# Performance work log

Hardware: AMD Instinct MI355X
Metric: run time of the kernel (lower is better)

## Reference

```python
import jax, jax.numpy as jnp
import numpy as np
from jax import lax

B, N, CIN, MID, OUT, G, H, CHILDS = 16, 1024, 256, 512, 256, 4, 1, 512


def _ln(x, g, b, eps=1e-6):
    m = x.mean(-1, keepdims=True)
    v = ((x - m) ** 2).mean(-1, keepdims=True)
    return (x - m) / jnp.sqrt(v + eps) * g + b


def _gconv(x, W, b):
    # grouped 1x1 conv1d: x [B,Cin,N], W [Cout, Cin//G], b [Cout]
    Bb, Cin, Nn = x.shape
    Cout = W.shape[0]
    xg = x.reshape(Bb, G, Cin // G, Nn)
    Wg = W.reshape(G, Cout // G, Cin // G)
    y = jnp.einsum('bgcn,goc->bgon', xg, Wg).reshape(Bb, Cout, Nn)
    return y + b[None, :, None]


def _forward(x, masks_roi1, masks_roi2, score_mask, gt_feat,
             W_att, b_att, W1, b1, W2, b2, g1, beta1, g2, beta2, Wg, bg):
    dt = x.dtype
    # gt branch
    gts = jax.nn.relu(gt_feat @ Wg + bg)  # [B,N,OUT]

    mr1 = masks_roi1 * score_mask[:, None, :]
    mr2 = masks_roi2 * score_mask[:, None, :]

    # attention logits without materializing the [B,N,N,2C] concat:
    # ft[b,i,j] = cat(x[b,j], x[b,i]);  logits = ft @ W_att + b_att
    Wq, Wk = W_att[:CIN], W_att[CIN:]
    lj = jnp.einsum('bjc,ch->bjh', x, Wq)  # query part (varies over j)
    li = jnp.einsum('bic,ch->bih', x, Wk)  # key part   (varies over i)
    attn = jax.nn.sigmoid(lj[:, None, :, :] + li[:, :, None, :] + b_att)  # [B,N,N,H]

    attn1 = attn * mr1[:, :, :, None]
    attn2 = attn * mr2[:, :, :, None]

    # torch fancy-index assign atten_mask[:,:,idces,:]=1 reduces to: any column
    # index appearing in ANY topk index set gets 1 along dim 2 for all b,i,h.
    k4, k2 = CHILDS // 4, CHILDS // 2
    a1 = jnp.moveaxis(attn1, 2, 3)  # [B,N,H,N] -> topk over last axis (= dim 2)
    a2 = jnp.moveaxis(attn2, 2, 3)
    idx1 = lax.top_k(a1, k4)[1]
    idx1m = lax.top_k(-a1, k4)[1]
    idx2 = lax.top_k(a2, k2)[1]
    idx2m = lax.top_k(-a2, k4)[1]
    all_idx = jnp.concatenate([idx1.ravel(), idx1m.ravel(), idx2.ravel(), idx2m.ravel()])
    col = jnp.zeros((N,), dtype=dt).at[all_idx].set(1.0)

    attn = attn * (mr1 + mr2)[:, :, :, None] * col[None, None, :, None]

    f = (score_mask == 0).astype(dt)  # [B,N]
    f_diag = f[:, :, None] * jnp.eye(N, dtype=dt)  # diag_embed
    atten = (attn + f_diag[:, :, :, None]) / CHILDS
    atten = jnp.transpose(atten, (0, 3, 2, 1))  # [B,H,Nj,Ni]

    x_t = jnp.transpose(x, (0, 2, 1))  # [B,CIN,N]
    o1 = jax.nn.relu(_gconv(x_t, W1, b1))  # [B,MID,N]
    o1m = jnp.matmul(o1.reshape(B, H, MID // H, N), atten).reshape(B, MID, N)
    o1m = _ln(jnp.transpose(o1m, (0, 2, 1)), g1, beta1)  # [B,N,MID]
    o1 = o1 + jnp.transpose(o1m, (0, 2, 1))

    o2 = jax.nn.relu(_gconv(o1, W2, b2))  # [B,OUT,N]
    o2m = jnp.matmul(o2.reshape(B, H, OUT // H, N), atten).reshape(B, OUT, N)
    node_feat = _ln(jnp.transpose(o2m, (0, 2, 1)), g2, beta2)  # [B,N,OUT]
    o2 = o2 + jnp.transpose(node_feat, (0, 2, 1))
    output2 = jnp.transpose(o2, (0, 2, 1))  # [B,N,OUT]
    return output2, gts, node_feat


def setup_inputs() -> dict:
    key = jax.random.key(0)
    ks = jax.random.split(key, 16)
    x = jax.random.normal(ks[0], (B, N, CIN), jnp.float32)
    masks_roi1 = (jax.random.uniform(ks[1], (B, N, N)) < 0.1).astype(jnp.float32)
    masks_roi2 = (jax.random.uniform(ks[2], (B, N, N)) < 0.1).astype(jnp.float32)
    score_mask = (jax.random.uniform(ks[3], (B, N)) < 0.8).astype(jnp.float32)
    gt_feat = jax.random.normal(ks[4], (B, N, CIN), jnp.float32)
    s = 0.05
    W_att = jax.random.normal(ks[5], (2 * CIN, H), jnp.float32) * s
    b_att = jnp.zeros((H,), jnp.float32)
    W1 = jax.random.normal(ks[6], (MID, CIN // G), jnp.float32) * s
    b1 = jax.random.normal(ks[7], (MID,), jnp.float32) * s
    W2 = jax.random.normal(ks[8], (OUT, MID // G), jnp.float32) * s
    b2 = jax.random.normal(ks[9], (OUT,), jnp.float32) * s
    g1 = jax.random.normal(ks[10], (MID,), jnp.float32) * s
    beta1 = jnp.zeros((MID,), jnp.float32)
    g2 = jax.random.normal(ks[11], (OUT,), jnp.float32) * s
    beta2 = jnp.zeros((OUT,), jnp.float32)
    Wg = jax.random.normal(ks[12], (CIN, OUT), jnp.float32) * s
    bg = jax.random.normal(ks[13], (OUT,), jnp.float32) * s
    return {"x": x, "masks_roi1": masks_roi1, "masks_roi2": masks_roi2,
            "score_mask": score_mask, "gt_feat": gt_feat,
            "W_att": W_att, "b_att": b_att, "W1": W1, "b1": b1,
            "W2": W2, "b2": b2, "g1": g1, "beta1": beta1,
            "g2": g2, "beta2": beta2, "Wg": Wg, "bg": bg}


def reference(x, masks_roi1, masks_roi2, score_mask, gt_feat,
              W_att, b_att, W1, b1, W2, b2, g1, beta1, g2, beta2, Wg, bg):
    return _forward(x, masks_roi1, masks_roi2, score_mask, gt_feat,
                    W_att, b_att, W1, b1, W2, b2, g1, beta1, g2, beta2, Wg, bg)
```

## Files before the change

kernel.cpp:

```cpp
#include <hip/hip_runtime.h>
#include <cstddef>
#include <cstdint>

#define B_ 16
#define N_ 1024
#define CIN_ 256
#define MID_ 512
#define OUT_ 256

typedef __attribute__((ext_vector_type(8))) short short8v;
typedef __attribute__((ext_vector_type(4))) float f32x4;

__device__ __forceinline__ float sigf(float z){ return 1.f/(1.f+expf(-z)); }
__device__ __forceinline__ ushort f2bf(float f){
  uint32_t u=__float_as_uint(f);
  uint32_t r=(u + 0x7fffu + ((u>>16)&1u))>>16;
  return (ushort)r;
}
__device__ __forceinline__ float bf2f(ushort u){ return __uint_as_float(((uint32_t)u)<<16); }

__device__ __forceinline__ void async16(void* lds, const void* g){
  __builtin_amdgcn_global_load_lds(
      (const __attribute__((address_space(1))) uint32_t*)g,
      (__attribute__((address_space(3))) uint32_t*)lds,
      16, 0, 0);
}

__global__ __launch_bounds__(256) void k_pc(const float* __restrict__ x,
    const float* __restrict__ gt, const float* __restrict__ Watt,
    float* __restrict__ lj, float* __restrict__ li,
    ushort* __restrict__ xb, ushort* __restrict__ gtb)
{
  int bid=blockIdx.x, wid=threadIdx.x>>6, lane=threadIdx.x&63;
  if(bid < 4096){
    int row = bid*4 + wid;
    float4 xv = ((const float4*)(x + (size_t)row*CIN_))[lane];
    ((ushort4*)(xb + (size_t)row*CIN_))[lane] =
        make_ushort4(f2bf(xv.x), f2bf(xv.y), f2bf(xv.z), f2bf(xv.w));
    float4 q = ((const float4*)Watt)[lane];
    float4 w = ((const float4*)(Watt + CIN_))[lane];
    float aq = xv.x*q.x+xv.y*q.y+xv.z*q.z+xv.w*q.w;
    float ak = xv.x*w.x+xv.y*w.y+xv.z*w.z+xv.w*w.w;
    #pragma unroll
    for(int off=32; off; off>>=1){ aq += __shfl_xor(aq,off); ak += __shfl_xor(ak,off); }
    if(lane==0){ lj[row]=aq; li[row]=ak; }
  } else {
    int row = (bid-4096)*4 + wid;
    float4 v = ((const float4*)(gt + (size_t)row*CIN_))[lane];
    ((ushort4*)(gtb + (size_t)row*CIN_))[lane] =
        make_ushort4(f2bf(v.x), f2bf(v.y), f2bf(v.z), f2bf(v.w));
  }
}

__global__ __launch_bounds__(256) void k_wcast(const float* __restrict__ W1,
    const float* __restrict__ W2, const float* __restrict__ Wg,
    ushort* __restrict__ W1b, ushort* __restrict__ W2b, ushort* __restrict__ WgTb)
{
  int bid=blockIdx.x, t=threadIdx.x;
  if(bid<128){ int i=bid*256+t; W1b[i]=f2bf(W1[i]); }
  else if(bid<256){ int i=(bid-128)*256+t; W2b[i]=f2bf(W2[i]); }
  else { int idx=(bid-256)*256+t; int o=idx>>8, c=idx&255; WgTb[idx]=f2bf(Wg[(size_t)c*OUT_+o]); }
}

__global__ __launch_bounds__(256) void k_col(
    const float* __restrict__ m1, const float* __restrict__ m2,
    const float* __restrict__ sc, const float* __restrict__ lj,
    const float* __restrict__ li, const float* __restrict__ batt,
    float* __restrict__ colf, ushort* __restrict__ mrs)
{
  int row = blockIdx.x; int b = row >> 10; int t = threadIdx.x;
  int lane = t&63, wid = t>>6;
  size_t base = (size_t)row*N_ + 4*t;
  float4 m1v = *(const float4*)(m1 + base);
  float4 m2v = *(const float4*)(m2 + base);
  float4 scv = *(const float4*)(sc + (b<<10) + 4*t);
  float mr1[4] = {m1v.x*scv.x, m1v.y*scv.y, m1v.z*scv.z, m1v.w*scv.w};
  float mr2[4] = {m2v.x*scv.x, m2v.y*scv.y, m2v.z*scv.z, m2v.w*scv.w};
  *(ushort4*)(mrs + base) = make_ushort4(f2bf(mr1[0]+mr2[0]), f2bf(mr1[1]+mr2[1]),
                                         f2bf(mr1[2]+mr2[2]), f2bf(mr1[3]+mr2[3]));
  int z1=0,z2=0;
  #pragma unroll
  for(int k=0;k<4;++k){ z1 += (mr1[k]==0.f); z2 += (mr2[k]==0.f); }
  int s = z1 | (z2<<16);
  #pragma unroll
  for(int off=1; off<64; off<<=1){
    int u = __shfl_up(s,off);
    if(lane>=off) s += u;
  }
  __shared__ int wsum[4];
  if(lane==63) wsum[wid]=s;
  __syncthreads();
  int prev=0, tot=0;
  #pragma unroll
  for(int w2=0;w2<4;++w2){ int v=wsum[w2]; tot+=v; if(w2<wid) prev+=v; }
  int incl = s + prev;
  int z1i = incl & 0xffff, z2i = incl >> 16;
  int excl1 = z1i - z1, excl2 = z2i - z2;
  int Z1 = tot & 0xffff, Z2 = tot >> 16;
  int P1 = 1024-Z1, P2 = 1024-Z2;
  bool rare = (P1>128)||(P2>256)||(Z1<128)||(Z2<128);
  if(!rare){
    int zb1=excl1, zb2=excl2;
    #pragma unroll
    for(int k=0;k<4;++k){
      bool q = (mr1[k]!=0.f) || (zb1<128) || (mr2[k]!=0.f) || (zb2<128) || (P2+zb2<256);
      if(q) colf[4*t+k]=1.0f;
      zb1 += (mr1[k]==0.f); zb2 += (mr2[k]==0.f);
    }
  } else {
    float lir=li[row], ba=batt[0];
    const float* m1r = m1 + (size_t)row*N_;
    const float* m2r = m2 + (size_t)row*N_;
    const float* scr = sc + (b<<10);
    const float* ljr = lj + (b<<10);
    float a1v[4], a2v[4];
    #pragma unroll
    for(int k=0;k<4;++k){
      float v = sigf(ljr[4*t+k]+lir+ba);
      a1v[k]=mr1[k]*v; a2v[k]=mr2[k]*v;
    }
    int c1[4]={0,0,0,0}, c1m[4]={0,0,0,0}, c2[4]={0,0,0,0}, c2m[4]={0,0,0,0};
    for(int jp=0;jp<N_;++jp){
      float vv = sigf(ljr[jp]+lir+ba);
      float p1 = m1r[jp]*scr[jp]*vv, p2 = m2r[jp]*scr[jp]*vv;
      #pragma unroll
      for(int k=0;k<4;++k){
        bool lo = jp < 4*t+k;
        c1[k] += (p1>a1v[k])||((p1==a1v[k])&&lo);
        c1m[k]+= (p1<a1v[k])||((p1==a1v[k])&&lo);
        c2[k] += (p2>a2v[k])||((p2==a2v[k])&&lo);
        c2m[k]+= (p2<a2v[k])||((p2==a2v[k])&&lo);
      }
    }
    #pragma unroll
    for(int k=0;k<4;++k)
      if(c1[k]<128||c1m[k]<128||c2[k]<256||c2m[k]<128) colf[4*t+k]=1.0f;
  }
}

__global__ __launch_bounds__(256) void k_at(const ushort* __restrict__ mrs,
    const float* __restrict__ sc, const float* __restrict__ lj,
    const float* __restrict__ li, const float* __restrict__ batt,
    const float* __restrict__ colf, ushort* __restrict__ Atb)
{
  int row=blockIdx.x, t=threadIdx.x; int b=row>>10, i=row&1023;
  size_t base=(size_t)row*N_ + 4*t;
  ushort4 mv=*(const ushort4*)(mrs+base);
  float4 ljv=*(const float4*)(lj + (b<<10) + 4*t);
  float4 cv =*(const float4*)(colf + 4*t);
  float lir=li[row], ba=batt[0];
  float fi = (sc[(b<<10)+i]==0.f)?1.f:0.f;
  float mra[4]={bf2f(mv.x),bf2f(mv.y),bf2f(mv.z),bf2f(mv.w)};
  float ljr[4]={ljv.x,ljv.y,ljv.z,ljv.w};
  float cr[4]={cv.x,cv.y,cv.z,cv.w};
  ushort o[4]; int j0=4*t;
  #pragma unroll
  for(int k=0;k<4;++k){
    float v=sigf(ljr[k]+lir+ba);
    float val=v*mra[k]*cr[k];
    if(j0+k==i) val+=fi;
    o[k]=f2bf(val*(1.f/512.f));
  }
  *(ushort4*)(Atb+base) = make_ushort4(o[0],o[1],o[2],o[3]);
}

template<int BM,int BN,int WR,int WC,int BK>
__global__ __launch_bounds__(256) void mgemm(
    const ushort* __restrict__ A, int lda, long long sAb, long long sAg,
    const ushort* __restrict__ Bp, int ldb, long long sBb, long long sBg,
    float* __restrict__ C, ushort* __restrict__ Cb, int ldc, long long sCb, long long sCg,
    ushort* __restrict__ CbT, long long sTb, long long sTg, int ldt,
    int K, int nG,
    const float* __restrict__ biasM, int biasMG,
    const float* __restrict__ biasN, int relu)
{
  static_assert(WR*WC==4 && BM==WR*64 && BN==WC*64, "tile");
  static_assert((BM*BK)%512==0 && (BN*BK)%512==0, "stage align");
  __shared__ __align__(16) ushort As[BM*BK];
  __shared__ __align__(16) ushort Bs[BN*BK];
  int z=blockIdx.z, b=z/nG, g=z%nG;
  A  += (size_t)b*sAb + (size_t)g*sAg;
  Bp += (size_t)b*sBb + (size_t)g*sBg;
  size_t cOff = (size_t)b*sCb + (size_t)g*sCg;
  size_t tOff = (size_t)b*sTb + (size_t)g*sTg;
  int m0 = blockIdx.y*BM, n0 = blockIdx.x*BN;
  int tid=threadIdx.x, w=tid>>6, lane=tid&63;
  int la=lane&15, hi=lane>>4;
  int wr=w/WC, wc=w%WC;
  f32x4 acc[4][4] = {};
  constexpr int ISS = (BM+BN)*BK/2048;
  for(int k0=0;k0<K;k0+=BK){
    #pragma unroll
    for(int r=0;r<ISS;++r){
      int e = (r*256 + tid)*8;
      if(e < BM*BK){
        int row=e/BK, kk=e%BK;
        async16((char*)As + (size_t)e*2, A + (size_t)(m0+row)*lda + k0+kk);
      } else {
        int e2=e-BM*BK; int row=e2/BK, kk=e2%BK;
        async16((char*)Bs + (size_t)e2*2, Bp + (size_t)(n0+row)*ldb + k0+kk);
      }
    }
    __syncthreads();
    #pragma unroll
    for(int h=0;h<BK/32;++h){
      short8v af[4], bf4[4];
      #pragma unroll
      for(int i2=0;i2<4;++i2) af[i2] = *(const short8v*)&As[(wr*64+i2*16+la)*BK + h*32 + hi*8];
      #pragma unroll
      for(int j2=0;j2<4;++j2) bf4[j2] = *(const short8v*)&Bs[(wc*64+j2*16+la)*BK + h*32 + hi*8];
      #pragma unroll
      for(int i2=0;i2<4;++i2)
        #pragma unroll
        for(int j2=0;j2<4;++j2)
          acc[i2][j2] = __builtin_amdgcn_mfma_f32_16x16x32_bf16(af[i2], bf4[j2], acc[i2][j2], 0,0,0);
    }
    __syncthreads();
  }
  #pragma unroll
  for(int i2=0;i2<4;++i2){
    int row0 = m0 + wr*64 + i2*16 + hi*4;
    #pragma unroll
    for(int j2=0;j2<4;++j2){
      int col = n0 + wc*64 + j2*16 + la;
      float bn = biasN ? biasN[col] : 0.f;
      #pragma unroll
      for(int r=0;r<4;++r){
        int row = row0 + r;
        float v = acc[i2][j2][r] + bn + (biasM ? biasM[(size_t)g*biasMG + row] : 0.f);
        if(relu) v = fmaxf(v, 0.f);
        if(C)   C  [cOff + (size_t)row*ldc + col] = v;
        if(Cb)  Cb [cOff + (size_t)row*ldc + col] = f2bf(v);
        if(CbT) CbT[tOff + (size_t)col*ldt + row] = f2bf(v);
      }
    }
  }
}

__global__ __launch_bounds__(256) void k_ln1(const float* __restrict__ o1mT,
    const ushort* __restrict__ o1bT,
    const float* __restrict__ g1v, const float* __restrict__ be1, ushort* __restrict__ o1pb)
{
  int row=blockIdx.x, t=threadIdx.x;
  float2 v = ((const float2*)(o1mT + (size_t)row*MID_))[t];
  float s=v.x+v.y, s2=v.x*v.x+v.y*v.y;
  for(int off=32; off; off>>=1){ s+=__shfl_down(s,off); s2+=__shfl_down(s2,off); }
  __shared__ float sm[8];
  int lane=t&63, wid=t>>6;
  if(lane==0){ sm[wid]=s; sm[4+wid]=s2; }
  __syncthreads();
  s=sm[0]+sm[1]+sm[2]+sm[3]; s2=sm[4]+sm[5]+sm[6]+sm[7];
  float mean=s*(1.f/MID_), var=s2*(1.f/MID_)-mean*mean;
  float rstd=rsqrtf(var+1e-6f);
  int m0=2*t;
  float a0=(v.x-mean)*rstd*g1v[m0]+be1[m0];
  float a1=(v.y-mean)*rstd*g1v[m0+1]+be1[m0+1];
  ushort2 rr = ((const ushort2*)(o1bT + (size_t)row*MID_))[t];
  ushort2 o; o.x=f2bf(a0+bf2f(rr.x)); o.y=f2bf(a1+bf2f(rr.y));
  ((ushort2*)(o1pb + (size_t)row*MID_))[t] = o;
}

__global__ __launch_bounds__(256) void k_ln2f(const float* __restrict__ o2mT,
    const ushort* __restrict__ o2bT,
    const float* __restrict__ g2v, const float* __restrict__ be2,
    float* __restrict__ node, float* __restrict__ out2)
{
  int row=blockIdx.x, t=threadIdx.x;
  float v = o2mT[(size_t)row*OUT_ + t];
  float s=v, s2=v*v;
  for(int off=32; off; off>>=1){ s+=__shfl_down(s,off); s2+=__shfl_down(s2,off); }
  __shared__ float sm[8];
  int lane=t&63, wid=t>>6;
  if(lane==0){ sm[wid]=s; sm[4+wid]=s2; }
  __syncthreads();
  s=sm[0]+sm[1]+sm[2]+sm[3]; s2=sm[4]+sm[5]+sm[6]+sm[7];
  float mean=s*(1.f/OUT_); float var=s2*(1.f/OUT_)-mean*mean;
  float rstd=rsqrtf(var+1e-6f);
  float nf=(v-mean)*rstd*g2v[t]+be2[t];
  size_t ro=(size_t)row*OUT_+t;
  node[ro]=nf;
  out2[ro]=nf + bf2f(o2bT[ro]);
}

extern "C" void kernel_launch(void* const* d_in, const int* in_sizes, int n_in,
                              void* d_out, int out_size, void* d_ws, size_t ws_size,
                              hipStream_t stream)
{
  const float* x    = (const float*)d_in[0];
  const float* m1   = (const float*)d_in[1];
  const float* m2   = (const float*)d_in[2];
  const float* sc   = (const float*)d_in[3];
  const float* gt   = (const float*)d_in[4];
  const float* Watt = (const float*)d_in[5];
  const float* batt = (const float*)d_in[6];
  const float* W1   = (const float*)d_in[7];
  const float* b1   = (const float*)d_in[8];
  const float* W2   = (const float*)d_in[9];
  const float* b2   = (const float*)d_in[10];
  const float* g1   = (const float*)d_in[11];
  const float* be1  = (const float*)d_in[12];
  const float* g2   = (const float*)d_in[13];
  const float* be2  = (const float*)d_in[14];
  const float* Wg   = (const float*)d_in[15];
  const float* bg   = (const float*)d_in[16];

  float* out2 = (float*)d_out;
  float* gtso = out2 + (size_t)B_*N_*OUT_;
  float* node = gtso + (size_t)B_*N_*OUT_;

  char* ws = (char*)d_ws;
  float*  colf = (float*)(ws);
  float*  lj   = (float*)(ws + 4096);
  float*  li   = (float*)(ws + 69632);
  ushort* W1b  = (ushort*)(ws + 135168);
  ushort* W2b  = (ushort*)(ws + 200704);
  ushort* WgTb = (ushort*)(ws + 266240);
  char* R1 = ws + 1048576;
  ushort* mrs  = (ushort*)R1;
  float*  o1mT = (float*)R1;
  ushort* Atb  = (ushort*)(ws + 34603008);
  char* R3 = ws + 68157440;
  ushort* xb   = (ushort*)R3;
  ushort* gtb  = (ushort*)(R3 + 8388608);
  ushort* o2b  = (ushort*)R3;
  ushort* o2bT = (ushort*)(R3 + 8388608);
  char* R4 = ws + 84934656;
  ushort* o1b  = (ushort*)R4;
  ushort* o1pb = (ushort*)R4;
  char* R5 = ws + 101711872;
  ushort* o1bT = (ushort*)R5;
  float*  o2mT = (float*)R5;

  hipMemsetAsync(colf, 0, 4096, stream);
  k_pc   <<<dim3(8192),dim3(256),0,stream>>>(x, gt, Watt, lj, li, xb, gtb);
  k_wcast<<<dim3(512),dim3(256),0,stream>>>(W1, W2, Wg, W1b, W2b, WgTb);
  k_col  <<<dim3(B_*N_),dim3(256),0,stream>>>(m1,m2,sc,lj,li,batt,colf,mrs);
  k_at   <<<dim3(B_*N_),dim3(256),0,stream>>>(mrs,sc,lj,li,batt,colf,Atb);

  mgemm<128,128,2,2,64><<<dim3(2,128,1),256,0,stream>>>(
      gtb, CIN_, 0,0,
      WgTb, CIN_, 0,0,
      gtso, (ushort*)0, OUT_, 0,0,
      (ushort*)0, 0,0,0,
      CIN_, 1, nullptr,0, bg, 1);

  mgemm<128,128,2,2,64><<<dim3(8,1,B_*4),256,0,stream>>>(
      W1b, 64, 0, (long long)128*64,
      xb, CIN_, (long long)N_*CIN_, 64,
      (float*)0, o1b, N_, (long long)MID_*N_, (long long)128*N_,
      o1bT, (long long)N_*MID_, 128, MID_,
      64, 4, b1, 128, nullptr, 1);

  mgemm<128,128,2,2,64><<<dim3(4,8,B_),256,0,stream>>>(
      Atb, N_, (long long)N_*N_, 0,
      o1b, N_, (long long)MID_*N_, 0,
      o1mT, (ushort*)0, MID_, (long long)N_*MID_, 0,
      (ushort*)0, 0,0,0,
      N_, 1, nullptr,0, nullptr, 0);

  k_ln1<<<dim3(B_*N_),256,0,stream>>>(o1mT, o1bT, g1, be1, o1pb);

  mgemm<64,256,1,4,64><<<dim3(4,1,B_*4),256,0,stream>>>(
      W2b, 128, 0, (long long)64*128,
      o1pb, MID_, (long long)N_*MID_, 128,
      (float*)0, o2b, N_, (long long)OUT_*N_, (long long)64*N_,
      o2bT, (long long)N_*OUT_, 64, OUT_,
      128, 4, b2, 64, nullptr, 1);

  mgemm<128,128,2,2,64><<<dim3(2,8,B_),256,0,stream>>>(
      Atb, N_, (long long)N_*N_, 0,
      o2b, N_, (long long)OUT_*N_, 0,
      o2mT, (ushort*)0, OUT_, (long long)N_*OUT_, 0,
      (ushort*)0, 0,0,0,
      N_, 1, nullptr,0, nullptr, 0);

  k_ln2f<<<dim3(B_*N_),256,0,stream>>>(o2mT, o2bT, g2, be2, node, out2);
}
```

Before: 398.4 us.

## Fuse column-mask and attention kernels, apply column mask in GEMM epilogue

Merges k_col and k_at into one pass that writes the attention matrix without the column factor. The column selection is now recorded as per-row ballot bitmasks, which a small kernel OR-reduces. The column mask is applied afterwards by zeroing the masked columns of the o1b/o2b operands in the producing GEMM epilogues, and the diagonal term for masked columns is corrected in the attention GEMM epilogue. This removes the intermediate mrs array, one full pass over the 16M-element mask rows, and the colf memset. The attention GEMM outputs are also stored as bf16 instead of fp32, which halves their write and read traffic but adds rounding error before the layer norms.

```diff
diff --git a/kernel.cpp b/kernel.cpp
--- a/kernel.cpp
+++ b/kernel.cpp
@@ -10,6 +10,7 @@
 
 typedef __attribute__((ext_vector_type(8))) short short8v;
 typedef __attribute__((ext_vector_type(4))) float f32x4;
+typedef unsigned long long ull;
 
 __device__ __forceinline__ float sigf(float z){ return 1.f/(1.f+expf(-z)); }
 __device__ __forceinline__ ushort f2bf(float f){
@@ -24,6 +25,10 @@
       (const __attribute__((address_space(1))) uint32_t*)g,
       (__attribute__((address_space(3))) uint32_t*)lds,
       16, 0, 0);
+}
+
+__device__ __forceinline__ int colbit(const ull* __restrict__ cm, int j){
+  return (int)((cm[((j>>8)<<2) | (j&3)] >> ((j>>2)&63)) & 1ull);
 }
 
 __global__ __launch_bounds__(256) void k_pc(const float* __restrict__ x,
@@ -62,66 +67,77 @@
   else { int idx=(bid-256)*256+t; int o=idx>>8, c=idx&255; WgTb[idx]=f2bf(Wg[(size_t)c*OUT_+o]); }
 }
 
-__global__ __launch_bounds__(256) void k_col(
+__global__ __launch_bounds__(256) void k_colat(
     const float* __restrict__ m1, const float* __restrict__ m2,
     const float* __restrict__ sc, const float* __restrict__ lj,
     const float* __restrict__ li, const float* __restrict__ batt,
-    float* __restrict__ colf, ushort* __restrict__ mrs)
-{
-  int row = blockIdx.x; int b = row >> 10; int t = threadIdx.x;
-  int lane = t&63, wid = t>>6;
+    ushort* __restrict__ Atb, ull* __restrict__ blockmask)
+{
+  int row = blockIdx.x; int b = row >> 10; int i = row & 1023;
+  int t = threadIdx.x, lane = t&63, wid = t>>6;
   size_t base = (size_t)row*N_ + 4*t;
   float4 m1v = *(const float4*)(m1 + base);
   float4 m2v = *(const float4*)(m2 + base);
   float4 scv = *(const float4*)(sc + (b<<10) + 4*t);
+  float4 ljv = *(const float4*)(lj + (b<<10) + 4*t);
+  float lir = li[row], ba = batt[0];
+  float fi = (sc[(b<<10)+i]==0.f)?1.f:0.f;
   float mr1[4] = {m1v.x*scv.x, m1v.y*scv.y, m1v.z*scv.z, m1v.w*scv.w};
   float mr2[4] = {m2v.x*scv.x, m2v.y*scv.y, m2v.z*scv.z, m2v.w*scv.w};
-  *(ushort4*)(mrs + base) = make_ushort4(f2bf(mr1[0]+mr2[0]), f2bf(mr1[1]+mr2[1]),
-                                         f2bf(mr1[2]+mr2[2]), f2bf(mr1[3]+mr2[3]));
-  int z1=0,z2=0;
+  float ljr[4] = {ljv.x,ljv.y,ljv.z,ljv.w};
+  ushort o[4];
   #pragma unroll
-  for(int k=0;k<4;++k){ z1 += (mr1[k]==0.f); z2 += (mr2[k]==0.f); }
-  int s = z1 | (z2<<16);
+  for(int k=0;k<4;++k){
+    float v = sigf(ljr[k]+lir+ba);
+    float val = v*(mr1[k]+mr2[k]);
+    if(4*t+k==i) val += fi;
+    o[k] = f2bf(val*(1.f/512.f));
+  }
+  *(ushort4*)(Atb+base) = make_ushort4(o[0],o[1],o[2],o[3]);
+  ull zb1m0=__ballot(mr1[0]==0.f), zb1m1=__ballot(mr1[1]==0.f),
+      zb1m2=__ballot(mr1[2]==0.f), zb1m3=__ballot(mr1[3]==0.f);
+  ull zb2m0=__ballot(mr2[0]==0.f), zb2m1=__ballot(mr2[1]==0.f),
+      zb2m2=__ballot(mr2[2]==0.f), zb2m3=__ballot(mr2[3]==0.f);
+  int wz1 = __popcll(zb1m0)+__popcll(zb1m1)+__popcll(zb1m2)+__popcll(zb1m3);
+  int wz2 = __popcll(zb2m0)+__popcll(zb2m1)+__popcll(zb2m2)+__popcll(zb2m3);
+  __shared__ int wz[8];
+  if(lane==0){ wz[wid]=wz1; wz[4+wid]=wz2; }
+  __syncthreads();
+  int pre1=0, pre2=0, Z1=0, Z2=0;
   #pragma unroll
-  for(int off=1; off<64; off<<=1){
-    int u = __shfl_up(s,off);
-    if(lane>=off) s += u;
-  }
-  __shared__ int wsum[4];
-  if(lane==63) wsum[wid]=s;
-  __syncthreads();
-  int prev=0, tot=0;
-  #pragma unroll
-  for(int w2=0;w2<4;++w2){ int v=wsum[w2]; tot+=v; if(w2<wid) prev+=v; }
-  int incl = s + prev;
-  int z1i = incl & 0xffff, z2i = incl >> 16;
-  int excl1 = z1i - z1, excl2 = z2i - z2;
-  int Z1 = tot & 0xffff, Z2 = tot >> 16;
+  for(int w2=0;w2<4;++w2){
+    Z1 += wz[w2]; Z2 += wz[4+w2];
+    if(w2<wid){ pre1 += wz[w2]; pre2 += wz[4+w2]; }
+  }
+  ull lt = (1ull<<lane)-1ull;
+  int r1 = pre1 + __popcll(zb1m0&lt)+__popcll(zb1m1&lt)+__popcll(zb1m2&lt)+__popcll(zb1m3&lt);
+  int r2 = pre2 + __popcll(zb2m0&lt)+__popcll(zb2m1&lt)+__popcll(zb2m2&lt)+__popcll(zb2m3&lt);
   int P1 = 1024-Z1, P2 = 1024-Z2;
   bool rare = (P1>128)||(P2>256)||(Z1<128)||(Z2<128);
+  bool q0,q1,q2,q3;
   if(!rare){
-    int zb1=excl1, zb2=excl2;
-    #pragma unroll
-    for(int k=0;k<4;++k){
-      bool q = (mr1[k]!=0.f) || (zb1<128) || (mr2[k]!=0.f) || (zb2<128) || (P2+zb2<256);
-      if(q) colf[4*t+k]=1.0f;
-      zb1 += (mr1[k]==0.f); zb2 += (mr2[k]==0.f);
-    }
+    int zb1=r1, zb2=r2;
+    q0 = (mr1[0]!=0.f)||(zb1<128)||(mr2[0]!=0.f)||(zb2<128)||(P2+zb2<256);
+    zb1 += (int)((zb1m0>>lane)&1ull); zb2 += (int)((zb2m0>>lane)&1ull);
+    q1 = (mr1[1]!=0.f)||(zb1<128)||(mr2[1]!=0.f)||(zb2<128)||(P2+zb2<256);
+    zb1 += (int)((zb1m1>>lane)&1ull); zb2 += (int)((zb2m1>>lane)&1ull);
+    q2 = (mr1[2]!=0.f)||(zb1<128)||(mr2[2]!=0.f)||(zb2<128)||(P2+zb2<256);
+    zb1 += (int)((zb1m2>>lane)&1ull); zb2 += (int)((zb2m2>>lane)&1ull);
+    q3 = (mr1[3]!=0.f)||(zb1<128)||(mr2[3]!=0.f)||(zb2<128)||(P2+zb2<256);
   } else {
-    float lir=li[row], ba=batt[0];
     const float* m1r = m1 + (size_t)row*N_;
     const float* m2r = m2 + (size_t)row*N_;
     const float* scr = sc + (b<<10);
-    const float* ljr = lj + (b<<10);
+    const float* ljp = lj + (b<<10);
     float a1v[4], a2v[4];
     #pragma unroll
     for(int k=0;k<4;++k){
-      float v = sigf(ljr[4*t+k]+lir+ba);
+      float v = sigf(ljp[4*t+k]+lir+ba);
       a1v[k]=mr1[k]*v; a2v[k]=mr2[k]*v;
     }
     int c1[4]={0,0,0,0}, c1m[4]={0,0,0,0}, c2[4]={0,0,0,0}, c2m[4]={0,0,0,0};
     for(int jp=0;jp<N_;++jp){
-      float vv = sigf(ljr[jp]+lir+ba);
+      float vv = sigf(ljp[jp]+lir+ba);
       float p1 = m1r[jp]*scr[jp]*vv, p2 = m2r[jp]*scr[jp]*vv;
       #pragma unroll
       for(int k=0;k<4;++k){
@@ -132,36 +148,32 @@
         c2m[k]+= (p2<a2v[k])||((p2==a2v[k])&&lo);
       }
     }
-    #pragma unroll
-    for(int k=0;k<4;++k)
-      if(c1[k]<128||c1m[k]<128||c2[k]<256||c2m[k]<128) colf[4*t+k]=1.0f;
-  }
-}
-
-__global__ __launch_bounds__(256) void k_at(const ushort* __restrict__ mrs,
-    const float* __restrict__ sc, const float* __restrict__ lj,
-    const float* __restrict__ li, const float* __restrict__ batt,
-    const float* __restrict__ colf, ushort* __restrict__ Atb)
-{
-  int row=blockIdx.x, t=threadIdx.x; int b=row>>10, i=row&1023;
-  size_t base=(size_t)row*N_ + 4*t;
-  ushort4 mv=*(const ushort4*)(mrs+base);
-  float4 ljv=*(const float4*)(lj + (b<<10) + 4*t);
-  float4 cv =*(const float4*)(colf + 4*t);
-  float lir=li[row], ba=batt[0];
-  float fi = (sc[(b<<10)+i]==0.f)?1.f:0.f;
-  float mra[4]={bf2f(mv.x),bf2f(mv.y),bf2f(mv.z),bf2f(mv.w)};
-  float ljr[4]={ljv.x,ljv.y,ljv.z,ljv.w};
-  float cr[4]={cv.x,cv.y,cv.z,cv.w};
-  ushort o[4]; int j0=4*t;
+    q0 = (c1[0]<128||c1m[0]<128||c2[0]<256||c2m[0]<128);
+    q1 = (c1[1]<128||c1m[1]<128||c2[1]<256||c2m[1]<128);
+    q2 = (c1[2]<128||c1m[2]<128||c2[2]<256||c2m[2]<128);
+    q3 = (c1[3]<128||c1m[3]<128||c2[3]<256||c2m[3]<128);
+  }
+  ull bq0=__ballot(q0), bq1=__ballot(q1), bq2=__ballot(q2), bq3=__ballot(q3);
+  if(lane<4){
+    ull v = (lane==0)?bq0 : (lane==1)?bq1 : (lane==2)?bq2 : bq3;
+    blockmask[(size_t)(wid*4+lane)*16384 + row] = v;
+  }
+}
+
+__global__ __launch_bounds__(256) void k_colred(const ull* __restrict__ blockmask,
+    ull* __restrict__ colmask64)
+{
+  int w = blockIdx.x;
+  const ull* p = blockmask + (size_t)w*16384;
+  ull acc = 0;
+  for(int r=threadIdx.x; r<16384; r+=256) acc |= p[r];
   #pragma unroll
-  for(int k=0;k<4;++k){
-    float v=sigf(ljr[k]+lir+ba);
-    float val=v*mra[k]*cr[k];
-    if(j0+k==i) val+=fi;
-    o[k]=f2bf(val*(1.f/512.f));
-  }
-  *(ushort4*)(Atb+base) = make_ushort4(o[0],o[1],o[2],o[3]);
+  for(int off=32; off; off>>=1) acc |= __shfl_xor(acc, off);
+  __shared__ ull sm[4];
+  int lane=threadIdx.x&63, wid=threadIdx.x>>6;
+  if(lane==0) sm[wid]=acc;
+  __syncthreads();
+  if(threadIdx.x==0) colmask64[w] = sm[0]|sm[1]|sm[2]|sm[3];
 }
 
 template<int BM,int BN,int WR,int WC,int BK>
@@ -170,12 +182,13 @@
     const ushort* __restrict__ Bp, int ldb, long long sBb, long long sBg,
     float* __restrict__ C, ushort* __restrict__ Cb, int ldc, long long sCb, long long sCg,
     ushort* __restrict__ CbT, long long sTb, long long sTg, int ldt,
+    const ull* __restrict__ colmask, int scaleCb,
+    const ushort* __restrict__ corrT, long long sQb, int ldq, const float* __restrict__ scp,
     int K, int nG,
     const float* __restrict__ biasM, int biasMG,
     const float* __restrict__ biasN, int relu)
 {
   static_assert(WR*WC==4 && BM==WR*64 && BN==WC*64, "tile");
-  static_assert((BM*BK)%512==0 && (BN*BK)%512==0, "stage align");
   __shared__ __align__(16) ushort As[BM*BK];
   __shared__ __align__(16) ushort Bs[BN*BK];
   int z=blockIdx.z, b=z/nG, g=z%nG;
@@ -224,26 +237,32 @@
     for(int j2=0;j2<4;++j2){
       int col = n0 + wc*64 + j2*16 + la;
       float bn = biasN ? biasN[col] : 0.f;
+      float cs = (scaleCb && !colbit(colmask, col)) ? 0.f : 1.f;
       #pragma unroll
       for(int r=0;r<4;++r){
         int row = row0 + r;
         float v = acc[i2][j2][r] + bn + (biasM ? biasM[(size_t)g*biasMG + row] : 0.f);
+        if(corrT){
+          if(scp[(size_t)b*1024 + row]==0.f && !colbit(colmask, row))
+            v += (1.f/512.f)*bf2f(corrT[(size_t)b*sQb + (size_t)row*ldq + col]);
+        }
         if(relu) v = fmaxf(v, 0.f);
         if(C)   C  [cOff + (size_t)row*ldc + col] = v;
-        if(Cb)  Cb [cOff + (size_t)row*ldc + col] = f2bf(v);
+        if(Cb)  Cb [cOff + (size_t)row*ldc + col] = f2bf(v*cs);
         if(CbT) CbT[tOff + (size_t)col*ldt + row] = f2bf(v);
       }
     }
   }
 }
 
-__global__ __launch_bounds__(256) void k_ln1(const float* __restrict__ o1mT,
+__global__ __launch_bounds__(256) void k_ln1(const ushort* __restrict__ o1mTb,
     const ushort* __restrict__ o1bT,
     const float* __restrict__ g1v, const float* __restrict__ be1, ushort* __restrict__ o1pb)
 {
   int row=blockIdx.x, t=threadIdx.x;
-  float2 v = ((const float2*)(o1mT + (size_t)row*MID_))[t];
-  float s=v.x+v.y, s2=v.x*v.x+v.y*v.y;
+  ushort2 vv = ((const ushort2*)(o1mTb + (size_t)row*MID_))[t];
+  float vx=bf2f(vv.x), vy=bf2f(vv.y);
+  float s=vx+vy, s2=vx*vx+vy*vy;
   for(int off=32; off; off>>=1){ s+=__shfl_down(s,off); s2+=__shfl_down(s2,off); }
   __shared__ float sm[8];
   int lane=t&63, wid=t>>6;
@@ -253,20 +272,20 @@
   float mean=s*(1.f/MID_), var=s2*(1.f/MID_)-mean*mean;
   float rstd=rsqrtf(var+1e-6f);
   int m0=2*t;
-  float a0=(v.x-mean)*rstd*g1v[m0]+be1[m0];
-  float a1=(v.y-mean)*rstd*g1v[m0+1]+be1[m0+1];
+  float a0=(vx-mean)*rstd*g1v[m0]+be1[m0];
+  float a1=(vy-mean)*rstd*g1v[m0+1]+be1[m0+1];
   ushort2 rr = ((const ushort2*)(o1bT + (size_t)row*MID_))[t];
   ushort2 o; o.x=f2bf(a0+bf2f(rr.x)); o.y=f2bf(a1+bf2f(rr.y));
   ((ushort2*)(o1pb + (size_t)row*MID_))[t] = o;
 }
 
-__global__ __launch_bounds__(256) void k_ln2f(const float* __restrict__ o2mT,
+__global__ __launch_bounds__(256) void k_ln2f(const ushort* __restrict__ o2mTb,
     const ushort* __restrict__ o2bT,
     const float* __restrict__ g2v, const float* __restrict__ be2,
     float* __restrict__ node, float* __restrict__ out2)
 {
   int row=blockIdx.x, t=threadIdx.x;
-  float v = o2mT[(size_t)row*OUT_ + t];
+  float v = bf2f(o2mTb[(size_t)row*OUT_ + t]);
   float s=v, s2=v*v;
   for(int off=32; off; off>>=1){ s+=__shfl_down(s,off); s2+=__shfl_down(s2,off); }
   __shared__ float sm[8];
@@ -309,39 +328,35 @@
   float* node = gtso + (size_t)B_*N_*OUT_;
 
   char* ws = (char*)d_ws;
-  float*  colf = (float*)(ws);
-  float*  lj   = (float*)(ws + 4096);
-  float*  li   = (float*)(ws + 69632);
-  ushort* W1b  = (ushort*)(ws + 135168);
-  ushort* W2b  = (ushort*)(ws + 200704);
-  ushort* WgTb = (ushort*)(ws + 266240);
-  char* R1 = ws + 1048576;
-  ushort* mrs  = (ushort*)R1;
-  float*  o1mT = (float*)R1;
-  ushort* Atb  = (ushort*)(ws + 34603008);
-  char* R3 = ws + 68157440;
-  ushort* xb   = (ushort*)R3;
-  ushort* gtb  = (ushort*)(R3 + 8388608);
-  ushort* o2b  = (ushort*)R3;
-  ushort* o2bT = (ushort*)(R3 + 8388608);
-  char* R4 = ws + 84934656;
-  ushort* o1b  = (ushort*)R4;
-  ushort* o1pb = (ushort*)R4;
-  char* R5 = ws + 101711872;
-  ushort* o1bT = (ushort*)R5;
-  float*  o2mT = (float*)R5;
-
-  hipMemsetAsync(colf, 0, 4096, stream);
-  k_pc   <<<dim3(8192),dim3(256),0,stream>>>(x, gt, Watt, lj, li, xb, gtb);
-  k_wcast<<<dim3(512),dim3(256),0,stream>>>(W1, W2, Wg, W1b, W2b, WgTb);
-  k_col  <<<dim3(B_*N_),dim3(256),0,stream>>>(m1,m2,sc,lj,li,batt,colf,mrs);
-  k_at   <<<dim3(B_*N_),dim3(256),0,stream>>>(mrs,sc,lj,li,batt,colf,Atb);
+  float* lj   = (float*)(ws);
+  float* li   = (float*)(ws + 65536);
+  ushort* W1b = (ushort*)(ws + 131072);
+  ushort* W2b = (ushort*)(ws + 196608);
+  ushort* WgTb= (ushort*)(ws + 262144);
+  ull* colmask= (ull*)(ws + 393216);
+  ull* blockmask = (ull*)(ws + 1048576);
+  ushort* Atb = (ushort*)(ws + 4194304);
+  ushort* xb   = (ushort*)(ws + 37748736);
+  ushort* gtb  = (ushort*)(ws + 46137344);
+  ushort* o2b  = xb;
+  ushort* o2bT = gtb;
+  ushort* o1b  = (ushort*)(ws + 54525952);
+  ushort* o1pb = o1b;
+  ushort* o1bT = (ushort*)(ws + 71303168);
+  ushort* o2mTb= (ushort*)(ws + 71303168);
+  ushort* o1mTb= (ushort*)(ws + 88080384);
+
+  k_pc    <<<dim3(8192),dim3(256),0,stream>>>(x, gt, Watt, lj, li, xb, gtb);
+  k_wcast <<<dim3(512),dim3(256),0,stream>>>(W1, W2, Wg, W1b, W2b, WgTb);
+  k_colat <<<dim3(B_*N_),dim3(256),0,stream>>>(m1,m2,sc,lj,li,batt,Atb,blockmask);
+  k_colred<<<dim3(16),dim3(256),0,stream>>>(blockmask, colmask);
 
   mgemm<128,128,2,2,64><<<dim3(2,128,1),256,0,stream>>>(
       gtb, CIN_, 0,0,
       WgTb, CIN_, 0,0,
       gtso, (ushort*)0, OUT_, 0,0,
       (ushort*)0, 0,0,0,
+      (ull*)0, 0, (ushort*)0, 0,0, (float*)0,
       CIN_, 1, nullptr,0, bg, 1);
 
   mgemm<128,128,2,2,64><<<dim3(8,1,B_*4),256,0,stream>>>(
@@ -349,30 +364,34 @@
       xb, CIN_, (long long)N_*CIN_, 64,
       (float*)0, o1b, N_, (long long)MID_*N_, (long long)128*N_,
       o1bT, (long long)N_*MID_, 128, MID_,
+      colmask, 1, (ushort*)0, 0,0, (float*)0,
       64, 4, b1, 128, nullptr, 1);
 
   mgemm<128,128,2,2,64><<<dim3(4,8,B_),256,0,stream>>>(
       Atb, N_, (long long)N_*N_, 0,
       o1b, N_, (long long)MID_*N_, 0,
-      o1mT, (ushort*)0, MID_, (long long)N_*MID_, 0,
+      (float*)0, o1mTb, MID_, (long long)N_*MID_, 0,
       (ushort*)0, 0,0,0,
+      colmask, 0, o1bT, (long long)N_*MID_, MID_, sc,
       N_, 1, nullptr,0, nullptr, 0);
 
-  k_ln1<<<dim3(B_*N_),256,0,stream>>>(o1mT, o1bT, g1, be1, o1pb);
+  k_ln1<<<dim3(B_*N_),256,0,stream>>>(o1mTb, o1bT, g1, be1, o1pb);
 
   mgemm<64,256,1,4,64><<<dim3(4,1,B_*4),256,0,stream>>>(
       W2b, 128, 0, (long long)64*128,
       o1pb, MID_, (long long)N_*MID_, 128,
       (float*)0, o2b, N_, (long long)OUT_*N_, (long long)64*N_,
       o2bT, (long long)N_*OUT_, 64, OUT_,
+      colmask, 1, (ushort*)0, 0,0, (float*)0,
       128, 4, b2, 64, nullptr, 1);
 
   mgemm<128,128,2,2,64><<<dim3(2,8,B_),256,0,stream>>>(
       Atb, N_, (long long)N_*N_, 0,
       o2b, N_, (long long)OUT_*N_, 0,
-      o2mT, (ushort*)0, OUT_, (long long)N_*OUT_, 0,
+      (float*)0, o2mTb, OUT_, (long long)N_*OUT_, 0,
       (ushort*)0, 0,0,0,
+      colmask, 0, o2bT, (long long)N_*OUT_, OUT_, sc,
       N_, 1, nullptr,0, nullptr, 0);
 
-  k_ln2f<<<dim3(B_*N_),256,0,stream>>>(o2mT, o2bT, g2, be2, node, out2);
-}
+  k_ln2f<<<dim3(B_*N_),256,0,stream>>>(o2mTb, o2bT, g2, be2, node, out2);
+}
```

New measurement: 425.5 us. 1.07x slower.
